# Performance work log

Measured on AMD Instinct MI355X. Metric: run time of the kernel, lower is better.

## Reference

```python
import jax, jax.numpy as jnp
import numpy as np

G = 56          # voxel grid resolution per axis
N = 65536
K = 27          # 3x3x3 kernel offsets
C_IN = 128
C_OUT = 128


def _build_rulebook():
    """Submanifold conv rulebook: for each kernel offset, (input_row, output_row) pairs.

    Padded to P=N pairs per offset; invalid pairs use in_idx=0 and out_idx=N
    (a dummy output slot that is dropped), so shapes are static.
    """
    rng = np.random.default_rng(0)
    keys = np.sort(rng.choice(G ** 3, size=N, replace=False)).astype(np.int64)
    x = keys // (G * G)
    y = (keys // G) % G
    z = keys % G
    in_idx = np.zeros((K, N), dtype=np.int32)
    out_idx = np.full((K, N), N, dtype=np.int32)
    k = 0
    for dx in (-1, 0, 1):
        for dy in (-1, 0, 1):
            for dz in (-1, 0, 1):
                nx, ny, nz = x + dx, y + dy, z + dz
                valid = (nx >= 0) & (nx < G) & (ny >= 0) & (ny < G) & (nz >= 0) & (nz < G)
                nkey = (nx * G + ny) * G + nz
                pos = np.searchsorted(keys, np.clip(nkey, 0, G ** 3 - 1))
                pos = np.clip(pos, 0, N - 1)
                found = valid & (keys[pos] == nkey)
                cnt = int(found.sum())
                in_idx[k, :cnt] = pos[found]
                out_idx[k, :cnt] = np.nonzero(found)[0]
                k += 1
    return jnp.asarray(in_idx), jnp.asarray(out_idx)


def setup_inputs() -> dict:
    key = jax.random.key(0)
    k1, k2, k3 = jax.random.split(key, 3)
    fan_in = K * C_IN
    features = jax.random.normal(k1, (N, C_IN), dtype=jnp.float32)
    weight = jax.random.normal(k2, (K, C_IN, C_OUT), dtype=jnp.float32) * (1.0 / np.sqrt(fan_in))
    bias = jax.random.normal(k3, (C_OUT,), dtype=jnp.float32) * 0.01
    in_idx, out_idx = _build_rulebook()
    return {"features": features, "weight": weight, "bias": bias,
            "in_idx": in_idx, "out_idx": out_idx}


def reference(features, weight, bias, in_idx, out_idx):
    # gather: [K, P, C_in]
    gathered = features[in_idx]
    # per-offset GEMM: [K, P, C_out]
    contrib = jnp.einsum('kpc,kcd->kpd', gathered, weight)
    n = features.shape[0]
    c_out = weight.shape[-1]
    # scatter-accumulate into N real rows + 1 dummy row for padded pairs
    out = jnp.zeros((n + 1, c_out), dtype=features.dtype)
    out = out.at[out_idx.reshape(-1)].add(contrib.reshape(-1, c_out))
    return out[:n] + bias
```

## Files before the change

kernel.cpp:

```cpp
#include <hip/hip_runtime.h>
#include <hip/hip_bf16.h>
#include <stdint.h>

#define NV   65536
#define KOFF 27
#define CIN  128
#define COUT 128

typedef __bf16 bf16x8 __attribute__((ext_vector_type(8)));
typedef float  f32x4  __attribute__((ext_vector_type(4)));

__device__ __forceinline__ void async_copy16(void* lds, const void* g) {
    __builtin_amdgcn_global_load_lds(
        (const __attribute__((address_space(1))) void*)g,
        (__attribute__((address_space(3))) void*)lds,
        16, 0, 0);
}

#define JOB_A_BLOCKS 4097
#define JOB_B_BLOCKS 216
#define JOB_S_BLOCKS 1728

__global__ void k_prep_all(const float* __restrict__ f,
                           uint4* __restrict__ fb4,
                           const float* __restrict__ w,
                           uint4* __restrict__ wfrag4,
                           const int4* __restrict__ in4,
                           const int4* __restrict__ out4,
                           int* __restrict__ nbr) {
    const int b = blockIdx.x;
    const int t = threadIdx.x;
    if (b < JOB_A_BLOCKS) {
        int i = b * 256 + t;
        int total8  = (NV + 1) * CIN / 8;
        int nvalid8 = NV * CIN / 8;
        if (i >= total8) return;
        union { uint4 u; __hip_bfloat16 h[8]; } p;
        if (i < nvalid8) {
            const float4* f4 = (const float4*)f;
            float4 a = f4[i * 2];
            float4 c = f4[i * 2 + 1];
            p.h[0] = __float2bfloat16(a.x);
            p.h[1] = __float2bfloat16(a.y);
            p.h[2] = __float2bfloat16(a.z);
            p.h[3] = __float2bfloat16(a.w);
            p.h[4] = __float2bfloat16(c.x);
            p.h[5] = __float2bfloat16(c.y);
            p.h[6] = __float2bfloat16(c.z);
            p.h[7] = __float2bfloat16(c.w);
        } else {
            p.u = make_uint4(0, 0, 0, 0);
        }
        fb4[i] = p.u;
    } else if (b < JOB_A_BLOCKS + JOB_B_BLOCKS) {
        int c    = (b - JOB_A_BLOCKS) * 256 + t;
        int lane = c & 63;
        int nt   = (c >> 6) & 1;
        int ks   = (c >> 7) & 3;
        int wv   = (c >> 9) & 3;
        int k    = c >> 11;
        int cout = wv * 32 + nt * 16 + (lane & 15);
        int cin0 = ks * 32 + (lane >> 4) * 8;
        const float* wk = w + k * 16384;
        union { uint4 u; __hip_bfloat16 h[8]; } p;
        #pragma unroll
        for (int j = 0; j < 8; ++j)
            p.h[j] = __float2bfloat16(wk[(cin0 + j) * 128 + cout]);
        wfrag4[c] = p.u;
    } else {
        int i = (b - JOB_A_BLOCKS - JOB_B_BLOCKS) * 256 + t;
        int k = i >> 14;
        int4 ii = in4[i];
        int4 oo = out4[i];
        int* nb = nbr + k * (NV + 1);
        nb[oo.x] = ii.x;
        nb[oo.y] = ii.y;
        nb[oo.z] = ii.z;
        nb[oo.w] = ii.w;
    }
}

__global__ __launch_bounds__(256, 2)
void sp_conv_main(const __hip_bfloat16* __restrict__ feats,
                  const uint4* __restrict__ wfrag,
                  const int* __restrict__ nbr,
                  const float* __restrict__ bias,
                  float* __restrict__ out) {
    __shared__ unsigned char smem[65536];

    const int t   = threadIdx.x;
    const int bid = blockIdx.x;
    const int tile0 = ((bid & 7) * 64 + (bid >> 3)) * 128;

    const int w    = t >> 6;
    const int lane = t & 63;
    const int lr   = lane & 15;
    const int quad = lane >> 4;

    const int srow   = t >> 4;
    const int sbyte  = ((t & 15) ^ srow) * 16;

    f32x4 acc[8][2] = {};

    const unsigned char* featsB = (const unsigned char*)feats;

    int arows[8];
    {
        const int* nbr0 = nbr + tile0;
        #pragma unroll
        for (int i = 0; i < 8; ++i) arows[i] = nbr0[i * 16 + srow];
    }
    #pragma unroll
    for (int i = 0; i < 8; ++i) {
        unsigned ar = min((unsigned)arows[i], (unsigned)NV);
        async_copy16(smem + i * 4096 + t * 16,
                     featsB + (size_t)ar * 256 + sbyte);
    }
    {
        const int* nbr1 = nbr + (NV + 1) + tile0;
        #pragma unroll
        for (int i = 0; i < 8; ++i) arows[i] = nbr1[i * 16 + srow];
    }
    uint4 bcur[4][2], bnext[4][2];
    {
        const uint4* wf0 = wfrag + w * 512 + lane;
        #pragma unroll
        for (int ks = 0; ks < 4; ++ks)
            #pragma unroll
            for (int nt = 0; nt < 2; ++nt)
                bcur[ks][nt] = wf0[ks * 128 + nt * 64];
    }
    __syncthreads();

    int cbuf = 0;
    for (int k = 0; k < KOFF; ++k) {
        if (k + 1 < KOFF) {
            unsigned char* dst = smem + (cbuf ^ 1) * 32768;
            #pragma unroll
            for (int i = 0; i < 8; ++i) {
                unsigned ar = min((unsigned)arows[i], (unsigned)NV);
                async_copy16(dst + i * 4096 + t * 16,
                             featsB + (size_t)ar * 256 + sbyte);
            }
            if (k + 2 < KOFF) {
                const int* nbrn = nbr + (k + 2) * (NV + 1) + tile0;
                #pragma unroll
                for (int i = 0; i < 8; ++i) arows[i] = nbrn[i * 16 + srow];
            }
            const uint4* wfn = wfrag + (k + 1) * 2048 + w * 512 + lane;
            #pragma unroll
            for (int ks = 0; ks < 4; ++ks)
                #pragma unroll
                for (int nt = 0; nt < 2; ++nt)
                    bnext[ks][nt] = wfn[ks * 128 + nt * 64];
        }

        const unsigned char* base = smem + cbuf * 32768;
        #pragma unroll
        for (int ks = 0; ks < 4; ++ks) {
            bf16x8 af[8];
            #pragma unroll
            for (int mt = 0; mt < 8; ++mt) {
                int row = mt * 16 + lr;
                af[mt] = *(const bf16x8*)(base + row * 256 +
                                          (((ks * 4 + quad) ^ lr) * 16));
            }
            #pragma unroll
            for (int mt = 0; mt < 8; ++mt)
                #pragma unroll
                for (int nt = 0; nt < 2; ++nt)
                    acc[mt][nt] = __builtin_amdgcn_mfma_f32_16x16x32_bf16(
                        af[mt], *(const bf16x8*)&bcur[ks][nt],
                        acc[mt][nt], 0, 0, 0);
        }
        __syncthreads();
        #pragma unroll
        for (int ks = 0; ks < 4; ++ks)
            #pragma unroll
            for (int nt = 0; nt < 2; ++nt)
                bcur[ks][nt] = bnext[ks][nt];
        cbuf ^= 1;
    }

    const int n0w = w * 32;
    float bv[2];
    #pragma unroll
    for (int nt = 0; nt < 2; ++nt) bv[nt] = bias[n0w + nt * 16 + lr];

    #pragma unroll
    for (int mt = 0; mt < 8; ++mt) {
        #pragma unroll
        for (int nt = 0; nt < 2; ++nt) {
            #pragma unroll
            for (int r = 0; r < 4; ++r) {
                int grow = tile0 + mt * 16 + quad * 4 + r;
                out[(size_t)grow * COUT + n0w + nt * 16 + lr] =
                    acc[mt][nt][r] + bv[nt];
            }
        }
    }
}


extern "C" void kernel_launch(void* const* d_in, const int* in_sizes, int n_in,
                              void* d_out, int out_size, void* d_ws, size_t ws_size,
                              hipStream_t stream) {
    const float* features = (const float*)d_in[0];
    const float* weight   = (const float*)d_in[1];
    const float* bias     = (const float*)d_in[2];
    const int*   in_idx   = (const int*)d_in[3];
    const int*   out_idx  = (const int*)d_in[4];
    float* out = (float*)d_out;

    uint8_t* ws = (uint8_t*)d_ws;
    size_t off = 0;
    __hip_bfloat16* feats_bf = (__hip_bfloat16*)(ws + off);
    off += (size_t)(NV + 1) * CIN * 2;
    off = (off + 255) & ~(size_t)255;
    uint4* wfrag = (uint4*)(ws + off);
    off += (size_t)KOFF * CIN * COUT * 2;
    off = (off + 255) & ~(size_t)255;
    int* nbr = (int*)(ws + off);

    hipMemsetAsync(nbr, 0xFF, (size_t)KOFF * (NV + 1) * 4, stream);

    k_prep_all<<<JOB_A_BLOCKS + JOB_B_BLOCKS + JOB_S_BLOCKS, 256, 0, stream>>>(
        features, (uint4*)feats_bf, weight, wfrag,
        (const int4*)in_idx, (const int4*)out_idx, nbr);

    sp_conv_main<<<NV / 128, 256, 0, stream>>>(feats_bf, wfrag, nbr, bias, out);
}
```

Before: 155.8 us.

## Interleave gather copies with per-k-slice MFMA phases using barriers and setprio

The 27-offset main loop is rewritten as an explicitly scheduled ping-pong. Each k-slice phase loads its A fragments from LDS and issues part of the next offset's async gather, index load or weight load. Warps then synchronize and run their MFMAs at raised priority. The loop is unrolled by two to swap weight register buffers without copies, and it waits with explicit vmcnt counts instead of full __syncthreads. The goal is better overlap of global gather latency and LDS reads with matrix math. In exchange it adds many more barriers per offset and relies on hand-counted vmcnt waits being correct.

```diff
diff --git a/kernel.cpp b/kernel.cpp
--- a/kernel.cpp
+++ b/kernel.cpp
@@ -97,14 +97,31 @@
     const int lr   = lane & 15;
     const int quad = lane >> 4;
 
-    const int srow   = t >> 4;
-    const int sbyte  = ((t & 15) ^ srow) * 16;
+    const int srow  = t >> 4;
+    const int sbyte = ((t & 15) ^ srow) * 16;
 
     f32x4 acc[8][2] = {};
 
     const unsigned char* featsB = (const unsigned char*)feats;
 
-    int arows[8];
+    int  arows[8];
+    uint4 bA[4][2], bB[4][2];
+
+    auto AFLOAD = [&](int rb, int ks, bf16x8 (&af)[8]) {
+        #pragma unroll
+        for (int mt = 0; mt < 8; ++mt)
+            af[mt] = *(const bf16x8*)(smem + rb + (mt * 16 + lr) * 256 +
+                                      (((ks * 4 + quad) ^ lr) * 16));
+    };
+    auto MFMA16 = [&](bf16x8 (&af)[8], uint4 (&b)[2]) {
+        #pragma unroll
+        for (int mt = 0; mt < 8; ++mt)
+            #pragma unroll
+            for (int nt = 0; nt < 2; ++nt)
+                acc[mt][nt] = __builtin_amdgcn_mfma_f32_16x16x32_bf16(
+                    af[mt], *(const bf16x8*)&b[nt], acc[mt][nt], 0, 0, 0);
+    };
+
     {
         const int* nbr0 = nbr + tile0;
         #pragma unroll
@@ -116,70 +133,114 @@
         async_copy16(smem + i * 4096 + t * 16,
                      featsB + (size_t)ar * 256 + sbyte);
     }
+    __builtin_amdgcn_sched_barrier(0);
     {
         const int* nbr1 = nbr + (NV + 1) + tile0;
         #pragma unroll
         for (int i = 0; i < 8; ++i) arows[i] = nbr1[i * 16 + srow];
     }
-    uint4 bcur[4][2], bnext[4][2];
     {
         const uint4* wf0 = wfrag + w * 512 + lane;
         #pragma unroll
         for (int ks = 0; ks < 4; ++ks)
             #pragma unroll
             for (int nt = 0; nt < 2; ++nt)
-                bcur[ks][nt] = wf0[ks * 128 + nt * 64];
-    }
-    __syncthreads();
-
-    int cbuf = 0;
-    for (int k = 0; k < KOFF; ++k) {
-        if (k + 1 < KOFF) {
-            unsigned char* dst = smem + (cbuf ^ 1) * 32768;
-            #pragma unroll
-            for (int i = 0; i < 8; ++i) {
+                bA[ks][nt] = wf0[ks * 128 + nt * 64];
+    }
+    asm volatile("s_waitcnt vmcnt(16)" ::: "memory");
+    __builtin_amdgcn_s_barrier();
+    __builtin_amdgcn_sched_barrier(0);
+
+    auto ITER = [&](int k, int rb, uint4 (&buse)[4][2], uint4 (&bload)[4][2]) {
+        const int sb = rb ^ 32768;
+
+        {
+            bf16x8 af[8];
+            AFLOAD(rb, 0, af);
+            #pragma unroll
+            for (int i = 0; i < 4; ++i) {
                 unsigned ar = min((unsigned)arows[i], (unsigned)NV);
-                async_copy16(dst + i * 4096 + t * 16,
+                async_copy16(smem + sb + i * 4096 + t * 16,
                              featsB + (size_t)ar * 256 + sbyte);
             }
-            if (k + 2 < KOFF) {
-                const int* nbrn = nbr + (k + 2) * (NV + 1) + tile0;
+            __builtin_amdgcn_s_barrier();
+            asm volatile("s_waitcnt lgkmcnt(0)" ::: "memory");
+            __builtin_amdgcn_sched_barrier(0);
+            __builtin_amdgcn_s_setprio(1);
+            MFMA16(af, buse[0]);
+            __builtin_amdgcn_s_setprio(0);
+            __builtin_amdgcn_s_barrier();
+            __builtin_amdgcn_sched_barrier(0);
+        }
+        {
+            bf16x8 af[8];
+            AFLOAD(rb, 1, af);
+            #pragma unroll
+            for (int i = 4; i < 8; ++i) {
+                unsigned ar = min((unsigned)arows[i], (unsigned)NV);
+                async_copy16(smem + sb + i * 4096 + t * 16,
+                             featsB + (size_t)ar * 256 + sbyte);
+            }
+            __builtin_amdgcn_s_barrier();
+            asm volatile("s_waitcnt lgkmcnt(0)" ::: "memory");
+            __builtin_amdgcn_sched_barrier(0);
+            __builtin_amdgcn_s_setprio(1);
+            MFMA16(af, buse[1]);
+            __builtin_amdgcn_s_setprio(0);
+            __builtin_amdgcn_s_barrier();
+            __builtin_amdgcn_sched_barrier(0);
+        }
+        {
+            bf16x8 af[8];
+            AFLOAD(rb, 2, af);
+            {
+                const int* nbrn = nbr + min(k + 2, KOFF - 1) * (NV + 1) + tile0;
                 #pragma unroll
                 for (int i = 0; i < 8; ++i) arows[i] = nbrn[i * 16 + srow];
             }
-            const uint4* wfn = wfrag + (k + 1) * 2048 + w * 512 + lane;
-            #pragma unroll
-            for (int ks = 0; ks < 4; ++ks)
+            __builtin_amdgcn_s_barrier();
+            asm volatile("s_waitcnt lgkmcnt(0)" ::: "memory");
+            __builtin_amdgcn_sched_barrier(0);
+            __builtin_amdgcn_s_setprio(1);
+            MFMA16(af, buse[2]);
+            __builtin_amdgcn_s_setprio(0);
+            __builtin_amdgcn_s_barrier();
+            __builtin_amdgcn_sched_barrier(0);
+        }
+        {
+            bf16x8 af[8];
+            AFLOAD(rb, 3, af);
+            {
+                const uint4* wfn = wfrag + (k + 1) * 2048 + w * 512 + lane;
                 #pragma unroll
-                for (int nt = 0; nt < 2; ++nt)
-                    bnext[ks][nt] = wfn[ks * 128 + nt * 64];
-        }
-
-        const unsigned char* base = smem + cbuf * 32768;
-        #pragma unroll
-        for (int ks = 0; ks < 4; ++ks) {
-            bf16x8 af[8];
-            #pragma unroll
-            for (int mt = 0; mt < 8; ++mt) {
-                int row = mt * 16 + lr;
-                af[mt] = *(const bf16x8*)(base + row * 256 +
-                                          (((ks * 4 + quad) ^ lr) * 16));
-            }
-            #pragma unroll
-            for (int mt = 0; mt < 8; ++mt)
-                #pragma unroll
-                for (int nt = 0; nt < 2; ++nt)
-                    acc[mt][nt] = __builtin_amdgcn_mfma_f32_16x16x32_bf16(
-                        af[mt], *(const bf16x8*)&bcur[ks][nt],
-                        acc[mt][nt], 0, 0, 0);
-        }
-        __syncthreads();
-        #pragma unroll
-        for (int ks = 0; ks < 4; ++ks)
-            #pragma unroll
-            for (int nt = 0; nt < 2; ++nt)
-                bcur[ks][nt] = bnext[ks][nt];
-        cbuf ^= 1;
+                for (int ks = 0; ks < 4; ++ks)
+                    #pragma unroll
+                    for (int nt = 0; nt < 2; ++nt)
+                        bload[ks][nt] = wfn[ks * 128 + nt * 64];
+            }
+            __builtin_amdgcn_s_barrier();
+            asm volatile("s_waitcnt lgkmcnt(0)" ::: "memory");
+            __builtin_amdgcn_sched_barrier(0);
+            __builtin_amdgcn_s_setprio(1);
+            MFMA16(af, buse[3]);
+            __builtin_amdgcn_s_setprio(0);
+            asm volatile("s_waitcnt vmcnt(16)" ::: "memory");
+            __builtin_amdgcn_s_barrier();
+            __builtin_amdgcn_sched_barrier(0);
+        }
+    };
+
+    #pragma unroll 1
+    for (int kk = 0; kk < KOFF - 1; kk += 2) {
+        ITER(kk,     0,     bA, bB);
+        ITER(kk + 1, 32768, bB, bA);
+    }
+
+    #pragma unroll
+    for (int ks = 0; ks < 4; ++ks) {
+        bf16x8 af[8];
+        AFLOAD(0, ks, af);
+        MFMA16(af, bA[ks]);
     }
 
     const int n0w = w * 32;
```

After: 151.8 us. 1.03x faster.

## Halve row tile to 64, raise occupancy, and fine-tune async pipeline waits

Applied to the files above, without the earlier changes.

Shrinks the per-block output tile from 128 to 64 voxel rows, which halves LDS use to 32 KB and the accumulator registers, and raises launch bounds to 4 blocks per CU with twice as many blocks launched. The k-loop is unrolled by two with ping-pong weight-fragment registers. The full __syncthreads is replaced by a partial vmcnt wait plus s_barrier, so weight prefetches stay in flight, and s_setprio is raised around the MFMA bursts. The intent is better latency hiding of the gather through occupancy and a finer-grained pipeline. In exchange each block reloads the full weight fragments for half as many rows, doubling weight traffic.

```diff
diff --git a/kernel.cpp b/kernel.cpp
--- a/kernel.cpp
+++ b/kernel.cpp
@@ -80,106 +80,115 @@
     }
 }
 
-__global__ __launch_bounds__(256, 2)
+__global__ __launch_bounds__(256, 4)
 void sp_conv_main(const __hip_bfloat16* __restrict__ feats,
                   const uint4* __restrict__ wfrag,
                   const int* __restrict__ nbr,
                   const float* __restrict__ bias,
                   float* __restrict__ out) {
-    __shared__ unsigned char smem[65536];
+    __shared__ unsigned char smem[32768];
 
     const int t   = threadIdx.x;
     const int bid = blockIdx.x;
-    const int tile0 = ((bid & 7) * 64 + (bid >> 3)) * 128;
+    const int tile0 = ((bid & 7) * 128 + (bid >> 3)) * 64;
 
     const int w    = t >> 6;
     const int lane = t & 63;
     const int lr   = lane & 15;
     const int quad = lane >> 4;
 
-    const int srow   = t >> 4;
-    const int sbyte  = ((t & 15) ^ srow) * 16;
-
-    f32x4 acc[8][2] = {};
+    const int srow  = t >> 4;
+    const int sbyte = ((t & 15) ^ srow) * 16;
+
+    f32x4 acc[4][2] = {};
 
     const unsigned char* featsB = (const unsigned char*)feats;
 
-    int arows[8];
+    int  arows[4];
+    uint4 bA[4][2], bB[4][2];
+
+    auto AFLOAD = [&](int rb, int ks, bf16x8 (&af)[4]) {
+        #pragma unroll
+        for (int mt = 0; mt < 4; ++mt)
+            af[mt] = *(const bf16x8*)(smem + rb + (mt * 16 + lr) * 256 +
+                                      (((ks * 4 + quad) ^ lr) * 16));
+    };
+    auto MFMA8 = [&](bf16x8 (&af)[4], uint4 (&b)[2]) {
+        #pragma unroll
+        for (int mt = 0; mt < 4; ++mt)
+            #pragma unroll
+            for (int nt = 0; nt < 2; ++nt)
+                acc[mt][nt] = __builtin_amdgcn_mfma_f32_16x16x32_bf16(
+                    af[mt], *(const bf16x8*)&b[nt], acc[mt][nt], 0, 0, 0);
+    };
+    auto BLOAD = [&](const uint4* wfk, uint4 (&b)[4][2]) {
+        #pragma unroll
+        for (int ks = 0; ks < 4; ++ks)
+            #pragma unroll
+            for (int nt = 0; nt < 2; ++nt)
+                b[ks][nt] = wfk[ks * 128 + nt * 64];
+    };
+    auto STAGE = [&](int sb) {
+        #pragma unroll
+        for (int i = 0; i < 4; ++i) {
+            unsigned ar = min((unsigned)arows[i], (unsigned)NV);
+            async_copy16(smem + sb + i * 4096 + t * 16,
+                         featsB + (size_t)ar * 256 + sbyte);
+        }
+    };
+
     {
         const int* nbr0 = nbr + tile0;
         #pragma unroll
-        for (int i = 0; i < 8; ++i) arows[i] = nbr0[i * 16 + srow];
-    }
-    #pragma unroll
-    for (int i = 0; i < 8; ++i) {
-        unsigned ar = min((unsigned)arows[i], (unsigned)NV);
-        async_copy16(smem + i * 4096 + t * 16,
-                     featsB + (size_t)ar * 256 + sbyte);
-    }
+        for (int i = 0; i < 4; ++i) arows[i] = nbr0[i * 16 + srow];
+    }
+    STAGE(0);
+    __builtin_amdgcn_sched_barrier(0);
     {
         const int* nbr1 = nbr + (NV + 1) + tile0;
         #pragma unroll
-        for (int i = 0; i < 8; ++i) arows[i] = nbr1[i * 16 + srow];
-    }
-    uint4 bcur[4][2], bnext[4][2];
-    {
-        const uint4* wf0 = wfrag + w * 512 + lane;
-        #pragma unroll
-        for (int ks = 0; ks < 4; ++ks)
-            #pragma unroll
-            for (int nt = 0; nt < 2; ++nt)
-                bcur[ks][nt] = wf0[ks * 128 + nt * 64];
-    }
-    __syncthreads();
-
-    int cbuf = 0;
-    for (int k = 0; k < KOFF; ++k) {
-        if (k + 1 < KOFF) {
-            unsigned char* dst = smem + (cbuf ^ 1) * 32768;
-            #pragma unroll
-            for (int i = 0; i < 8; ++i) {
-                unsigned ar = min((unsigned)arows[i], (unsigned)NV);
-                async_copy16(dst + i * 4096 + t * 16,
-                             featsB + (size_t)ar * 256 + sbyte);
-            }
-            if (k + 2 < KOFF) {
-                const int* nbrn = nbr + (k + 2) * (NV + 1) + tile0;
-                #pragma unroll
-                for (int i = 0; i < 8; ++i) arows[i] = nbrn[i * 16 + srow];
-            }
-            const uint4* wfn = wfrag + (k + 1) * 2048 + w * 512 + lane;
-            #pragma unroll
-            for (int ks = 0; ks < 4; ++ks)
-                #pragma unroll
-                for (int nt = 0; nt < 2; ++nt)
-                    bnext[ks][nt] = wfn[ks * 128 + nt * 64];
-        }
-
-        const unsigned char* base = smem + cbuf * 32768;
+        for (int i = 0; i < 4; ++i) arows[i] = nbr1[i * 16 + srow];
+    }
+    BLOAD(wfrag + w * 512 + lane, bA);
+    asm volatile("s_waitcnt vmcnt(12)" ::: "memory");
+    __builtin_amdgcn_s_barrier();
+    __builtin_amdgcn_sched_barrier(0);
+
+    auto ITER = [&](int k, int rb, uint4 (&buse)[4][2], uint4 (&bload)[4][2]) {
+        const int sb = rb ^ 16384;
+        STAGE(sb);
+        __builtin_amdgcn_sched_barrier(0);
+        {
+            const int* nbrn = nbr + min(k + 2, KOFF - 1) * (NV + 1) + tile0;
+            #pragma unroll
+            for (int i = 0; i < 4; ++i) arows[i] = nbrn[i * 16 + srow];
+        }
+        BLOAD(wfrag + (k + 1) * 2048 + w * 512 + lane, bload);
         #pragma unroll
         for (int ks = 0; ks < 4; ++ks) {
-            bf16x8 af[8];
-            #pragma unroll
-            for (int mt = 0; mt < 8; ++mt) {
-                int row = mt * 16 + lr;
-                af[mt] = *(const bf16x8*)(base + row * 256 +
-                                          (((ks * 4 + quad) ^ lr) * 16));
-            }
-            #pragma unroll
-            for (int mt = 0; mt < 8; ++mt)
-                #pragma unroll
-                for (int nt = 0; nt < 2; ++nt)
-                    acc[mt][nt] = __builtin_amdgcn_mfma_f32_16x16x32_bf16(
-                        af[mt], *(const bf16x8*)&bcur[ks][nt],
-                        acc[mt][nt], 0, 0, 0);
-        }
-        __syncthreads();
-        #pragma unroll
-        for (int ks = 0; ks < 4; ++ks)
-            #pragma unroll
-            for (int nt = 0; nt < 2; ++nt)
-                bcur[ks][nt] = bnext[ks][nt];
-        cbuf ^= 1;
+            bf16x8 af[4];
+            AFLOAD(rb, ks, af);
+            __builtin_amdgcn_s_setprio(1);
+            MFMA8(af, buse[ks]);
+            __builtin_amdgcn_s_setprio(0);
+        }
+        __builtin_amdgcn_sched_barrier(0);
+        asm volatile("s_waitcnt vmcnt(12)" ::: "memory");
+        __builtin_amdgcn_s_barrier();
+        __builtin_amdgcn_sched_barrier(0);
+    };
+
+    #pragma unroll 1
+    for (int kk = 0; kk < KOFF - 1; kk += 2) {
+        ITER(kk,     0,     bA, bB);
+        ITER(kk + 1, 16384, bB, bA);
+    }
+
+    #pragma unroll
+    for (int ks = 0; ks < 4; ++ks) {
+        bf16x8 af[4];
+        AFLOAD(0, ks, af);
+        MFMA8(af, bA[ks]);
     }
 
     const int n0w = w * 32;
@@ -188,7 +197,7 @@
     for (int nt = 0; nt < 2; ++nt) bv[nt] = bias[n0w + nt * 16 + lr];
 
     #pragma unroll
-    for (int mt = 0; mt < 8; ++mt) {
+    for (int mt = 0; mt < 4; ++mt) {
         #pragma unroll
         for (int nt = 0; nt < 2; ++nt) {
             #pragma unroll
@@ -228,5 +237,5 @@
         features, (uint4*)feats_bf, weight, wfrag,
         (const int4*)in_idx, (const int4*)out_idx, nbr);
 
-    sp_conv_main<<<NV / 128, 256, 0, stream>>>(feats_bf, wfrag, nbr, bias, out);
-}
+    sp_conv_main<<<NV / 64, 256, 0, stream>>>(feats_bf, wfrag, nbr, bias, out);
+}
```

New measurement: 176.3 us. +13.2%, slower.

## Stage contiguous input row windows per dx-group in LDS and gather via local indices

Applied to the files above, without the earlier changes.

Instead of gathering 128 neighbor rows into LDS for every one of the 27 offsets, each block loads one contiguous window of input rows per dx group (9 offsets). The window is bounded by the per-tile min/max input row, which an extra prep pass computes with atomics. The main loop then reads A fragments directly from LDS through 16-bit local indices, and invalid pairs point to a zeroed row. This cuts global gather traffic and barriers. The cost is an extra prep kernel and memsets, and it relies on each window fitting in 316 rows; rows beyond that are silently clamped, which holds for this sorted voxel layout but not in general.

```diff
diff --git a/kernel.cpp b/kernel.cpp
--- a/kernel.cpp
+++ b/kernel.cpp
@@ -6,6 +6,8 @@
 #define KOFF 27
 #define CIN  128
 #define COUT 128
+#define ZROW 316
+#define NROWS 320
 
 typedef __bf16 bf16x8 __attribute__((ext_vector_type(8)));
 typedef float  f32x4  __attribute__((ext_vector_type(4)));
@@ -19,15 +21,17 @@
 
 #define JOB_A_BLOCKS 4097
 #define JOB_B_BLOCKS 216
-#define JOB_S_BLOCKS 1728
-
-__global__ void k_prep_all(const float* __restrict__ f,
-                           uint4* __restrict__ fb4,
-                           const float* __restrict__ w,
-                           uint4* __restrict__ wfrag4,
-                           const int4* __restrict__ in4,
-                           const int4* __restrict__ out4,
-                           int* __restrict__ nbr) {
+#define JOB_R_BLOCKS 1728
+
+__global__ void k_prep1(const float* __restrict__ f,
+                        uint4* __restrict__ fb4,
+                        const float* __restrict__ w,
+                        uint4* __restrict__ wfrag4,
+                        const int4* __restrict__ in4,
+                        const int4* __restrict__ out4,
+                        int* __restrict__ rmin_a,
+                        int* __restrict__ rmax_a) {
+    __shared__ int smin[32], smax[32], stile[32];
     const int b = blockIdx.x;
     const int t = threadIdx.x;
     if (b < JOB_A_BLOCKS) {
@@ -70,117 +74,163 @@
     } else {
         int i = (b - JOB_A_BLOCKS - JOB_B_BLOCKS) * 256 + t;
         int k = i >> 14;
+        int g = k / 9;
+        if (t < 32) { smin[t] = 0x7FFFFFFF; smax[t] = -1; stile[t] = -1; }
+        __syncthreads();
         int4 ii = in4[i];
         int4 oo = out4[i];
-        int* nb = nbr + k * (NV + 1);
-        nb[oo.x] = ii.x;
-        nb[oo.y] = ii.y;
-        nb[oo.z] = ii.z;
-        nb[oo.w] = ii.w;
+        int ivals[4] = { ii.x, ii.y, ii.z, ii.w };
+        int ovals[4] = { oo.x, oo.y, oo.z, oo.w };
+        #pragma unroll
+        for (int j = 0; j < 4; ++j) {
+            int o = ovals[j];
+            if ((unsigned)o < NV) {
+                int tl = o >> 7, s = tl & 31;
+                stile[s] = tl;
+                atomicMin(&smin[s], ivals[j]);
+                atomicMax(&smax[s], ivals[j]);
+            }
+        }
+        __syncthreads();
+        if (t < 32) {
+            int tl = stile[t];
+            if (tl >= 0) {
+                atomicMin(&rmin_a[tl * 3 + g], smin[t]);
+                atomicMax(&rmax_a[tl * 3 + g], smax[t]);
+            }
+        }
+    }
+}
+
+__global__ void k_prep2(const int4* __restrict__ in4,
+                        const int4* __restrict__ out4,
+                        const int* __restrict__ rmin_a,
+                        unsigned short* __restrict__ lnbr16) {
+    int i = blockIdx.x * 256 + threadIdx.x;
+    int k = i >> 14;
+    int g = k / 9;
+    int4 ii = in4[i];
+    int4 oo = out4[i];
+    int ivals[4] = { ii.x, ii.y, ii.z, ii.w };
+    int ovals[4] = { oo.x, oo.y, oo.z, oo.w };
+    #pragma unroll
+    for (int j = 0; j < 4; ++j) {
+        int o = ovals[j];
+        if ((unsigned)o < NV) {
+            int tl = o >> 7;
+            int li = ivals[j] - rmin_a[tl * 3 + g];
+            lnbr16[((size_t)k << 16) + (tl << 7) + (o & 15) * 8 + ((o >> 4) & 7)]
+                = (unsigned short)li;
+        }
     }
 }
 
 __global__ __launch_bounds__(256, 2)
 void sp_conv_main(const __hip_bfloat16* __restrict__ feats,
                   const uint4* __restrict__ wfrag,
-                  const int* __restrict__ nbr,
+                  const unsigned short* __restrict__ lnbr16,
+                  const int* __restrict__ rmin_a,
+                  const int* __restrict__ rmax_a,
                   const float* __restrict__ bias,
                   float* __restrict__ out) {
-    __shared__ unsigned char smem[65536];
+    __shared__ unsigned char smem[NROWS * 256];
 
     const int t   = threadIdx.x;
     const int bid = blockIdx.x;
-    const int tile0 = ((bid & 7) * 64 + (bid >> 3)) * 128;
+    const int tile  = (bid & 7) * 64 + (bid >> 3);
+    const int tile0 = tile * 128;
 
     const int w    = t >> 6;
     const int lane = t & 63;
     const int lr   = lane & 15;
     const int quad = lane >> 4;
-
-    const int srow   = t >> 4;
-    const int sbyte  = ((t & 15) ^ srow) * 16;
+    const int srow = t >> 4;
 
     f32x4 acc[8][2] = {};
+    uint4 bX[4][2], bY[4][2];
+    uint4 lX, lY;
 
     const unsigned char* featsB = (const unsigned char*)feats;
 
-    int arows[8];
-    {
-        const int* nbr0 = nbr + tile0;
-        #pragma unroll
-        for (int i = 0; i < 8; ++i) arows[i] = nbr0[i * 16 + srow];
-    }
-    #pragma unroll
-    for (int i = 0; i < 8; ++i) {
-        unsigned ar = min((unsigned)arows[i], (unsigned)NV);
-        async_copy16(smem + i * 4096 + t * 16,
-                     featsB + (size_t)ar * 256 + sbyte);
-    }
-    {
-        const int* nbr1 = nbr + (NV + 1) + tile0;
-        #pragma unroll
-        for (int i = 0; i < 8; ++i) arows[i] = nbr1[i * 16 + srow];
-    }
-    uint4 bcur[4][2], bnext[4][2];
-    {
-        const uint4* wf0 = wfrag + w * 512 + lane;
+    if (t < 16) *(uint4*)(smem + ZROW * 256 + t * 16) = make_uint4(0, 0, 0, 0);
+
+    auto LLOAD = [&](int k, uint4& l) {
+        l = *(const uint4*)(lnbr16 + ((size_t)k << 16) + tile0 + lr * 8);
+    };
+    auto BLOADf = [&](const uint4* wfk, uint4 (&bf)[4][2]) {
         #pragma unroll
         for (int ks = 0; ks < 4; ++ks)
             #pragma unroll
             for (int nt = 0; nt < 2; ++nt)
-                bcur[ks][nt] = wf0[ks * 128 + nt * 64];
-    }
-    __syncthreads();
-
-    int cbuf = 0;
-    for (int k = 0; k < KOFF; ++k) {
-        if (k + 1 < KOFF) {
-            unsigned char* dst = smem + (cbuf ^ 1) * 32768;
-            #pragma unroll
-            for (int i = 0; i < 8; ++i) {
-                unsigned ar = min((unsigned)arows[i], (unsigned)NV);
-                async_copy16(dst + i * 4096 + t * 16,
-                             featsB + (size_t)ar * 256 + sbyte);
-            }
-            if (k + 2 < KOFF) {
-                const int* nbrn = nbr + (k + 2) * (NV + 1) + tile0;
-                #pragma unroll
-                for (int i = 0; i < 8; ++i) arows[i] = nbrn[i * 16 + srow];
-            }
-            const uint4* wfn = wfrag + (k + 1) * 2048 + w * 512 + lane;
-            #pragma unroll
-            for (int ks = 0; ks < 4; ++ks)
-                #pragma unroll
-                for (int nt = 0; nt < 2; ++nt)
-                    bnext[ks][nt] = wfn[ks * 128 + nt * 64];
-        }
-
-        const unsigned char* base = smem + cbuf * 32768;
+                bf[ks][nt] = wfk[ks * 128 + nt * 64];
+    };
+    auto MFMA16 = [&](bf16x8 (&af)[8], uint4 (&bf)[2]) {
+        #pragma unroll
+        for (int mt = 0; mt < 8; ++mt)
+            #pragma unroll
+            for (int nt = 0; nt < 2; ++nt)
+                acc[mt][nt] = __builtin_amdgcn_mfma_f32_16x16x32_bf16(
+                    af[mt], *(const bf16x8*)&bf[nt], acc[mt][nt], 0, 0, 0);
+    };
+    auto STEP = [&](int k, uint4& luse, uint4& lload,
+                    uint4 (&buse)[4][2], uint4 (&bload)[4][2]) {
+        int kn = min(k + 1, KOFF - 1);
+        LLOAD(kn, lload);
+        BLOADf(wfrag + kn * 2048 + w * 512 + lane, bload);
+        const unsigned short* ls = (const unsigned short*)&luse;
+        unsigned vb[8];
+        #pragma unroll
+        for (int mt = 0; mt < 8; ++mt) {
+            int li = min((int)ls[mt], ZROW);
+            vb[mt] = (unsigned)(li * 256 + ((quad << 4) ^ ((li & 15) << 4)));
+        }
         #pragma unroll
         for (int ks = 0; ks < 4; ++ks) {
             bf16x8 af[8];
             #pragma unroll
-            for (int mt = 0; mt < 8; ++mt) {
-                int row = mt * 16 + lr;
-                af[mt] = *(const bf16x8*)(base + row * 256 +
-                                          (((ks * 4 + quad) ^ lr) * 16));
-            }
-            #pragma unroll
             for (int mt = 0; mt < 8; ++mt)
-                #pragma unroll
-                for (int nt = 0; nt < 2; ++nt)
-                    acc[mt][nt] = __builtin_amdgcn_mfma_f32_16x16x32_bf16(
-                        af[mt], *(const bf16x8*)&bcur[ks][nt],
-                        acc[mt][nt], 0, 0, 0);
-        }
-        __syncthreads();
-        #pragma unroll
-        for (int ks = 0; ks < 4; ++ks)
-            #pragma unroll
-            for (int nt = 0; nt < 2; ++nt)
-                bcur[ks][nt] = bnext[ks][nt];
-        cbuf ^= 1;
-    }
+                af[mt] = *(const bf16x8*)(smem + (vb[mt] ^ (unsigned)(ks << 6)));
+            MFMA16(af, buse[ks]);
+        }
+    };
+    auto STAGEG = [&](int g) {
+        int rmn = rmin_a[tile * 3 + g];
+        int cnt = rmax_a[tile * 3 + g] - rmn + 1;
+        cnt = min(cnt, 316);
+        const unsigned char* src = featsB + (size_t)rmn * 256 +
+                                   (((t & 15) ^ srow) * 16);
+        #pragma unroll 1
+        for (int j = 0; j < 20; ++j) {
+            if (j * 16 >= cnt) break;
+            int row = j * 16 + srow;
+            if (row < cnt)
+                async_copy16(smem + row * 256 + (t & 15) * 16,
+                             src + (size_t)row * 256);
+        }
+    };
+    auto GROUP = [&](int g, uint4& lU, uint4& lV,
+                     uint4 (&bU)[4][2], uint4 (&bV)[4][2]) {
+        STAGEG(g);
+        __syncthreads();
+        const int k0 = g * 9;
+        STEP(k0 + 0, lU, lV, bU, bV);
+        STEP(k0 + 1, lV, lU, bV, bU);
+        STEP(k0 + 2, lU, lV, bU, bV);
+        STEP(k0 + 3, lV, lU, bV, bU);
+        STEP(k0 + 4, lU, lV, bU, bV);
+        STEP(k0 + 5, lV, lU, bV, bU);
+        STEP(k0 + 6, lU, lV, bU, bV);
+        STEP(k0 + 7, lV, lU, bV, bU);
+        STEP(k0 + 8, lU, lV, bU, bV);
+        __syncthreads();
+    };
+
+    LLOAD(0, lX);
+    BLOADf(wfrag + w * 512 + lane, bX);
+
+    GROUP(0, lX, lY, bX, bY);
+    GROUP(1, lY, lX, bY, bX);
+    GROUP(2, lX, lY, bX, bY);
 
     const int n0w = w * 32;
     float bv[2];
@@ -220,13 +270,25 @@
     uint4* wfrag = (uint4*)(ws + off);
     off += (size_t)KOFF * CIN * COUT * 2;
     off = (off + 255) & ~(size_t)255;
-    int* nbr = (int*)(ws + off);
-
-    hipMemsetAsync(nbr, 0xFF, (size_t)KOFF * (NV + 1) * 4, stream);
-
-    k_prep_all<<<JOB_A_BLOCKS + JOB_B_BLOCKS + JOB_S_BLOCKS, 256, 0, stream>>>(
+    unsigned short* lnbr16 = (unsigned short*)(ws + off);
+    off += (size_t)KOFF * NV * 2;
+    off = (off + 255) & ~(size_t)255;
+    int* rmin_a = (int*)(ws + off);
+    off += 512 * 3 * 4;
+    off = (off + 255) & ~(size_t)255;
+    int* rmax_a = (int*)(ws + off);
+
+    hipMemsetAsync(lnbr16, 0xFF, (size_t)KOFF * NV * 2, stream);
+    hipMemsetAsync(rmin_a, 0x7F, 512 * 3 * 4, stream);
+    hipMemsetAsync(rmax_a, 0x00, 512 * 3 * 4, stream);
+
+    k_prep1<<<JOB_A_BLOCKS + JOB_B_BLOCKS + JOB_R_BLOCKS, 256, 0, stream>>>(
         features, (uint4*)feats_bf, weight, wfrag,
-        (const int4*)in_idx, (const int4*)out_idx, nbr);
-
-    sp_conv_main<<<NV / 128, 256, 0, stream>>>(feats_bf, wfrag, nbr, bias, out);
-}
+        (const int4*)in_idx, (const int4*)out_idx, rmin_a, rmax_a);
+
+    k_prep2<<<JOB_R_BLOCKS, 256, 0, stream>>>(
+        (const int4*)in_idx, (const int4*)out_idx, rmin_a, lnbr16);
+
+    sp_conv_main<<<NV / 128, 256, 0, stream>>>(
+        feats_bf, wfrag, lnbr16, rmin_a, rmax_a, bias, out);
+}
```

New measurement: 164.4 us. +5.5%, slower.
